# Performance work log

Measured on AMD Instinct MI355X. Metric: run time of the kernel, lower is better.

Reference implementation:

```python
import jax, jax.numpy as jnp
import numpy as np

N_NODES = 100000
IN_CH, HID_CH, OUT_CH = 128, 128, 64
N_EDGES = 1600000


def _gcn_conv(x, W, b, src, dst, num_nodes):
    """PyG GCNConv with gcn_norm(add_self_loops=True): adds one self-loop per
    node to the given edge set, symmetric deg^-1/2 normalization, then
    gather-scale-scatter of the linearly transformed features."""
    loop = jnp.arange(num_nodes)
    s = jnp.concatenate([src, loop])
    d = jnp.concatenate([dst, loop])
    # degree over targets (flow source_to_target), edge weights = 1
    deg = jax.ops.segment_sum(jnp.ones_like(s, x.dtype), d, num_segments=num_nodes)
    dinv = jnp.where(deg > 0, deg ** -0.5, 0.0)
    norm = dinv[s] * dinv[d]                      # [E']
    h = x @ W                                     # [N, out]
    msg = h[s] * norm[:, None]                    # [E', out] gather + scale
    out = jax.ops.segment_sum(msg, d, num_segments=num_nodes)  # scatter-add
    return out + b


def setup_inputs() -> dict:
    key = jax.random.key(0)
    k = jax.random.split(key, 6)
    x = jax.random.normal(k[0], (N_NODES, IN_CH), dtype=jnp.float32)
    edge_index = jax.random.randint(k[1], (2, N_EDGES), 0, N_NODES, dtype=jnp.int64)
    # Glorot-scale params
    W1 = jax.random.normal(k[2], (IN_CH, HID_CH), dtype=jnp.float32) * (2.0 / (IN_CH + HID_CH)) ** 0.5
    b1 = jnp.zeros((HID_CH,), dtype=jnp.float32)
    W2 = jax.random.normal(k[3], (HID_CH, OUT_CH), dtype=jnp.float32) * (2.0 / (HID_CH + OUT_CH)) ** 0.5
    b2 = jnp.zeros((OUT_CH,), dtype=jnp.float32)
    return {"x": x, "edge_index": edge_index, "W1": W1, "b1": b1, "W2": W2, "b2": b2}


def reference(x, edge_index, W1, b1, W2, b2):
    num_nodes = x.shape[0]
    loop = jnp.arange(num_nodes, dtype=edge_index.dtype)
    # wrapper-level add_self_loops (GCNConv adds another internally)
    src = jnp.concatenate([edge_index[0], loop])
    dst = jnp.concatenate([edge_index[1], loop])
    h = _gcn_conv(x, W1, b1, src, dst, num_nodes)
    h = jax.nn.relu(h)
    h = _gcn_conv(h, W2, b2, src, dst, num_nodes)
    return jax.nn.log_softmax(h, axis=1)
```

## Files before the change

### kernel.cpp

```cpp
#include <hip/hip_runtime.h>
#include <cstdint>
#include <cstddef>

#define IN_CH 128
#define HID_CH 128
#define OUT_CH 64
#define BSH 8
#define PB 4096

typedef unsigned int uint32;
typedef unsigned char uchar;
typedef short bf16x8 __attribute__((ext_vector_type(8)));
typedef float f32x4 __attribute__((ext_vector_type(4)));
typedef float f32x2 __attribute__((ext_vector_type(2)));

static __device__ __forceinline__ unsigned short f2bf(float f) {
    uint32 u = __float_as_uint(f);
    u += 0x7fffu + ((u >> 16) & 1u);
    return (unsigned short)(u >> 16);
}
static __device__ __forceinline__ uchar f2fp8(float f) {
    int p = __builtin_amdgcn_cvt_pk_fp8_f32(f, f, 0, false);
    return (uchar)(p & 0xff);
}


__global__ __launch_bounds__(256) void bhist_wtrans(
    const int* __restrict__ dst, int* __restrict__ bcnt, int E, int NB, int gP,
    const float* __restrict__ W1, const float* __restrict__ W2,
    unsigned short* __restrict__ W1t, unsigned short* __restrict__ W2t) {
    if (blockIdx.x >= (uint32)gP) {
        int t = (blockIdx.x - gP) * 256 + threadIdx.x;
        if (t < 128 * 128) {
            int nc = t >> 7, k = t & 127;
            W1t[t] = f2bf(W1[k * 128 + nc]);
        }
        int u = t - 128 * 128;
        if (u >= 0 && u < 64 * 128) {
            int nc = u >> 7, k = u & 127;
            W2t[u] = f2bf(W2[k * 64 + nc]);
        }
        return;
    }
    __shared__ int h[512];
    int t = threadIdx.x;
    int e0 = blockIdx.x * PB;
    int cnt = min(PB, E - e0);
    for (int b = t; b < NB; b += 256) h[b] = 0;
    __syncthreads();
    for (int i = t; i < cnt; i += 256)
        atomicAdd(&h[dst[e0 + i] >> BSH], 1);
    __syncthreads();
    for (int b = t; b < NB; b += 256)
        if (h[b]) atomicAdd(&bcnt[b], h[b]);
}

__global__ void bscan(const int* __restrict__ bcnt, int* __restrict__ bbase,
                      int* __restrict__ bcur, int NB, int E) {
    __shared__ int s[512];
    int t = threadIdx.x;
    int v = (t < NB) ? bcnt[t] : 0;
    s[t] = v;
    __syncthreads();
    for (int o = 1; o < 512; o <<= 1) {
        int add = (t >= o) ? s[t - o] : 0;
        __syncthreads();
        s[t] += add;
        __syncthreads();
    }
    if (t < NB) { bbase[t] = s[t] - v; bcur[t] = 0; }
    if (t == 0) bbase[NB] = E;
}

__global__ __launch_bounds__(256) void part1(
    const int* __restrict__ src, const int* __restrict__ dst,
    const int* __restrict__ bbase, int* __restrict__ bcur,
    int2* __restrict__ pairBuf, int E, int NB) {
    __shared__ int2 pairs[PB];
    __shared__ int hist[512];
    __shared__ int base[512];
    int t = threadIdx.x;
    int e0 = blockIdx.x * PB;
    int cnt = min(PB, E - e0);
    for (int b = t; b < NB; b += 256) hist[b] = 0;
    __syncthreads();
    for (int i = t; i < cnt; i += 256) {
        int s = src[e0 + i], d = dst[e0 + i];
        pairs[i] = make_int2(s, d);
        atomicAdd(&hist[d >> BSH], 1);
    }
    __syncthreads();
    for (int b = t; b < NB; b += 256) {
        int h = hist[b];
        int gb = (h > 0) ? atomicAdd(&bcur[b], h) : 0;
        base[b] = bbase[b] + gb;
        hist[b] = 0;
    }
    __syncthreads();
    for (int i = t; i < cnt; i += 256) {
        int2 p = pairs[i];
        int b = p.y >> BSH;
        int q = base[b] + atomicAdd(&hist[b], 1);
        pairBuf[q] = p;
    }
}

__global__ __launch_bounds__(256) void bucket_build(
    const int2* __restrict__ pairBuf, const int* __restrict__ bbase,
    int* __restrict__ rowptr, int* __restrict__ deg, float* __restrict__ dinv,
    int* __restrict__ csr, int N) {
    __shared__ int cnt[256];
    __shared__ int loc[256];
    int b = blockIdx.x, t = threadIdx.x;
    int start = bbase[b], end = bbase[b + 1];
    cnt[t] = 0;
    __syncthreads();
    for (int i = start + t; i < end; i += 256)
        atomicAdd(&cnt[pairBuf[i].y & 255], 1);
    __syncthreads();
    int v = cnt[t];
    loc[t] = v;
    __syncthreads();
    for (int o = 1; o < 256; o <<= 1) {
        int add = (t >= o) ? loc[t - o] : 0;
        __syncthreads();
        loc[t] += add;
        __syncthreads();
    }
    int excl = loc[t] - v;
    int node = (b << BSH) + t;
    if (node < N) {
        rowptr[node] = start + excl;
        deg[node] = v;
        dinv[node] = rsqrtf((float)(v + 2));
    }
    __syncthreads();
    cnt[t] = excl;
    __syncthreads();
    for (int i = start + t; i < end; i += 256) {
        int2 p = pairBuf[i];
        int q = start + atomicAdd(&cnt[p.y & 255], 1);
        csr[q] = p.x;
    }
}


template <int OUT, bool AFP32>
__global__ __launch_bounds__(256) void gemm_mfma(
    const void* __restrict__ Av, const unsigned short* __restrict__ Wt,
    uchar* __restrict__ C, int n) {
    constexpr int AP = 72;
    constexpr int WP = 136;
    constexpr int NT = OUT / 16;
    __shared__ unsigned short As[128 * AP];
    __shared__ unsigned short Ws[OUT * WP];

    const int t = threadIdx.x;
    const int row0 = blockIdx.x * 128;

    for (int i = t; i < OUT * 16; i += 256) {
        int rr = i >> 4, sq = i & 15;
        *(uint4*)&Ws[rr * WP + sq * 8] = *(const uint4*)(Wt + rr * 128 + sq * 8);
    }

    const int w = t >> 6, l = t & 63;
    const int q = l >> 4, r16 = l & 15;
    const int mbase = w * 32;

    f32x4 acc0[NT], acc1[NT];
    for (int i = 0; i < NT; i++) {
        acc0[i] = (f32x4){0.f, 0.f, 0.f, 0.f};
        acc1[i] = (f32x4){0.f, 0.f, 0.f, 0.f};
    }

    for (int half = 0; half < 2; half++) {
        if (half) __syncthreads();
        if (AFP32) {
            const float* A = (const float*)Av;
            for (int i = t; i < 128 * 16; i += 256) {
                int rr = i >> 4, fq = i & 15;
                float4 v = make_float4(0.f, 0.f, 0.f, 0.f);
                if (row0 + rr < n)
                    v = *(const float4*)(A + (size_t)(row0 + rr) * 128 + half * 64 + fq * 4);
                unsigned short* p = &As[rr * AP + fq * 4];
                p[0] = f2bf(v.x); p[1] = f2bf(v.y); p[2] = f2bf(v.z); p[3] = f2bf(v.w);
            }
        } else {
            const unsigned short* A = (const unsigned short*)Av;
            for (int i = t; i < 128 * 8; i += 256) {
                int rr = i >> 3, sq = i & 7;
                uint4 v = make_uint4(0, 0, 0, 0);
                if (row0 + rr < n)
                    v = *(const uint4*)(A + (size_t)(row0 + rr) * 128 + half * 64 + sq * 8);
                *(uint4*)&As[rr * AP + sq * 8] = v;
            }
        }
        __syncthreads();

#pragma unroll
        for (int kc = 0; kc < 2; kc++) {
            int ko = kc * 32 + q * 8;
            int kow = half * 64 + ko;
            bf16x8 a0 = *(const bf16x8*)&As[(mbase + r16) * AP + ko];
            bf16x8 a1 = *(const bf16x8*)&As[(mbase + 16 + r16) * AP + ko];
#pragma unroll
            for (int nt = 0; nt < NT; nt++) {
                bf16x8 b = *(const bf16x8*)&Ws[(nt * 16 + r16) * WP + kow];
                acc0[nt] = __builtin_amdgcn_mfma_f32_16x16x32_bf16(a0, b, acc0[nt], 0, 0, 0);
                acc1[nt] = __builtin_amdgcn_mfma_f32_16x16x32_bf16(a1, b, acc1[nt], 0, 0, 0);
            }
        }
    }

#pragma unroll
    for (int nt = 0; nt < NT; nt++) {
#pragma unroll
        for (int p = 0; p < 4; p++) {
            int rr = row0 + mbase + q * 4 + p;
            if (rr < n) C[(size_t)rr * OUT + nt * 16 + r16] = f2fp8(acc0[nt][p]);
            if (rr + 16 < n) C[(size_t)(rr + 16) * OUT + nt * 16 + r16] = f2fp8(acc1[nt][p]);
        }
    }
}


__global__ __launch_bounds__(256) void agg_relu_128(
    const uchar* __restrict__ H, const int* __restrict__ csr,
    const int* __restrict__ rowptr, const int* __restrict__ deg,
    const float* __restrict__ dinv, const float* __restrict__ bias,
    unsigned short* __restrict__ out, int n) {
    int v = blockIdx.x * 16 + (threadIdx.x >> 4);
    int hl = threadIdx.x & 15;
    int gsel = threadIdx.x & 48;
    bool valid = v < n;
    int vc = valid ? v : 0;
    int base = rowptr[vc];
    int cnt = valid ? deg[vc] : 0;

    float4 aL0 = make_float4(0.f, 0.f, 0.f, 0.f), aH0 = aL0;
    float4 aL1 = aL0, aH1 = aL0, aL2 = aL0, aH2 = aL0, aL3 = aL0, aH3 = aL0;

    for (int j0 = 0; j0 < cnt; j0 += 16) {
        int nj = min(16, cnt - j0);
        int ul = 0; float wl = 0.f;
        if (hl < nj) { ul = csr[base + j0 + hl]; wl = dinv[ul]; }
        int j = 0;
        for (; j + 4 <= nj; j += 4) {
            int s0 = j | gsel, s1 = (j + 1) | gsel, s2 = (j + 2) | gsel, s3 = (j + 3) | gsel;
            int u0 = __shfl(ul, s0), u1 = __shfl(ul, s1);
            int u2 = __shfl(ul, s2), u3 = __shfl(ul, s3);
            float w0 = __shfl(wl, s0), w1 = __shfl(wl, s1);
            float w2 = __shfl(wl, s2), w3 = __shfl(wl, s3);
            uint2 h0 = *(const uint2*)(H + (size_t)u0 * 128 + hl * 8);
            uint2 h1 = *(const uint2*)(H + (size_t)u1 * 128 + hl * 8);
            uint2 h2 = *(const uint2*)(H + (size_t)u2 * 128 + hl * 8);
            uint2 h3 = *(const uint2*)(H + (size_t)u3 * 128 + hl * 8);
            {
                f32x2 p0 = __builtin_amdgcn_cvt_pk_f32_fp8(h0.x, false);
                f32x2 p1 = __builtin_amdgcn_cvt_pk_f32_fp8(h0.x, true);
                f32x2 p2 = __builtin_amdgcn_cvt_pk_f32_fp8(h0.y, false);
                f32x2 p3 = __builtin_amdgcn_cvt_pk_f32_fp8(h0.y, true);
                aL0.x += w0 * p0[0]; aL0.y += w0 * p0[1]; aL0.z += w0 * p1[0]; aL0.w += w0 * p1[1];
                aH0.x += w0 * p2[0]; aH0.y += w0 * p2[1]; aH0.z += w0 * p3[0]; aH0.w += w0 * p3[1];
            }
            {
                f32x2 p0 = __builtin_amdgcn_cvt_pk_f32_fp8(h1.x, false);
                f32x2 p1 = __builtin_amdgcn_cvt_pk_f32_fp8(h1.x, true);
                f32x2 p2 = __builtin_amdgcn_cvt_pk_f32_fp8(h1.y, false);
                f32x2 p3 = __builtin_amdgcn_cvt_pk_f32_fp8(h1.y, true);
                aL1.x += w1 * p0[0]; aL1.y += w1 * p0[1]; aL1.z += w1 * p1[0]; aL1.w += w1 * p1[1];
                aH1.x += w1 * p2[0]; aH1.y += w1 * p2[1]; aH1.z += w1 * p3[0]; aH1.w += w1 * p3[1];
            }
            {
                f32x2 p0 = __builtin_amdgcn_cvt_pk_f32_fp8(h2.x, false);
                f32x2 p1 = __builtin_amdgcn_cvt_pk_f32_fp8(h2.x, true);
                f32x2 p2 = __builtin_amdgcn_cvt_pk_f32_fp8(h2.y, false);
                f32x2 p3 = __builtin_amdgcn_cvt_pk_f32_fp8(h2.y, true);
                aL2.x += w2 * p0[0]; aL2.y += w2 * p0[1]; aL2.z += w2 * p1[0]; aL2.w += w2 * p1[1];
                aH2.x += w2 * p2[0]; aH2.y += w2 * p2[1]; aH2.z += w2 * p3[0]; aH2.w += w2 * p3[1];
            }
            {
                f32x2 p0 = __builtin_amdgcn_cvt_pk_f32_fp8(h3.x, false);
                f32x2 p1 = __builtin_amdgcn_cvt_pk_f32_fp8(h3.x, true);
                f32x2 p2 = __builtin_amdgcn_cvt_pk_f32_fp8(h3.y, false);
                f32x2 p3 = __builtin_amdgcn_cvt_pk_f32_fp8(h3.y, true);
                aL3.x += w3 * p0[0]; aL3.y += w3 * p0[1]; aL3.z += w3 * p1[0]; aL3.w += w3 * p1[1];
                aH3.x += w3 * p2[0]; aH3.y += w3 * p2[1]; aH3.z += w3 * p3[0]; aH3.w += w3 * p3[1];
            }
        }
        for (; j < nj; j++) {
            int s = j | gsel;
            int u = __shfl(ul, s);
            float wv = __shfl(wl, s);
            uint2 h = *(const uint2*)(H + (size_t)u * 128 + hl * 8);
            f32x2 p0 = __builtin_amdgcn_cvt_pk_f32_fp8(h.x, false);
            f32x2 p1 = __builtin_amdgcn_cvt_pk_f32_fp8(h.x, true);
            f32x2 p2 = __builtin_amdgcn_cvt_pk_f32_fp8(h.y, false);
            f32x2 p3 = __builtin_amdgcn_cvt_pk_f32_fp8(h.y, true);
            aL0.x += wv * p0[0]; aL0.y += wv * p0[1]; aL0.z += wv * p1[0]; aL0.w += wv * p1[1];
            aH0.x += wv * p2[0]; aH0.y += wv * p2[1]; aH0.z += wv * p3[0]; aH0.w += wv * p3[1];
        }
    }
    if (valid) {
        float4 aL = make_float4((aL0.x + aL1.x) + (aL2.x + aL3.x),
                                (aL0.y + aL1.y) + (aL2.y + aL3.y),
                                (aL0.z + aL1.z) + (aL2.z + aL3.z),
                                (aL0.w + aL1.w) + (aL2.w + aL3.w));
        float4 aH = make_float4((aH0.x + aH1.x) + (aH2.x + aH3.x),
                                (aH0.y + aH1.y) + (aH2.y + aH3.y),
                                (aH0.z + aH1.z) + (aH2.z + aH3.z),
                                (aH0.w + aH1.w) + (aH2.w + aH3.w));
        float dv = dinv[vc];
        float sl = 2.f * dv * dv;
        uint2 hv = *(const uint2*)(H + (size_t)vc * 128 + hl * 8);
        f32x2 s0 = __builtin_amdgcn_cvt_pk_f32_fp8(hv.x, false);
        f32x2 s1 = __builtin_amdgcn_cvt_pk_f32_fp8(hv.x, true);
        f32x2 s2 = __builtin_amdgcn_cvt_pk_f32_fp8(hv.y, false);
        f32x2 s3 = __builtin_amdgcn_cvt_pk_f32_fp8(hv.y, true);
        const float4* bp = (const float4*)(bias + hl * 8);
        float4 b0 = bp[0], b1 = bp[1];
        float o0 = fmaxf(dv * aL.x + sl * s0[0] + b0.x, 0.f);
        float o1 = fmaxf(dv * aL.y + sl * s0[1] + b0.y, 0.f);
        float o2 = fmaxf(dv * aL.z + sl * s1[0] + b0.z, 0.f);
        float o3 = fmaxf(dv * aL.w + sl * s1[1] + b0.w, 0.f);
        float o4 = fmaxf(dv * aH.x + sl * s2[0] + b1.x, 0.f);
        float o5 = fmaxf(dv * aH.y + sl * s2[1] + b1.y, 0.f);
        float o6 = fmaxf(dv * aH.z + sl * s3[0] + b1.z, 0.f);
        float o7 = fmaxf(dv * aH.w + sl * s3[1] + b1.w, 0.f);
        uint4 pk;
        pk.x = (uint32)f2bf(o0) | ((uint32)f2bf(o1) << 16);
        pk.y = (uint32)f2bf(o2) | ((uint32)f2bf(o3) << 16);
        pk.z = (uint32)f2bf(o4) | ((uint32)f2bf(o5) << 16);
        pk.w = (uint32)f2bf(o6) | ((uint32)f2bf(o7) << 16);
        *(uint4*)(out + (size_t)vc * 128 + hl * 8) = pk;
    }
}

__global__ __launch_bounds__(256) void agg_lsm_64(
    const uchar* __restrict__ H, const int* __restrict__ csr,
    const int* __restrict__ rowptr, const int* __restrict__ deg,
    const float* __restrict__ dinv, const float* __restrict__ bias,
    float* __restrict__ out, int n) {
    int v = blockIdx.x * 16 + (threadIdx.x >> 4);
    int hl = threadIdx.x & 15;
    int gsel = threadIdx.x & 48;
    bool valid = v < n;
    int vc = valid ? v : 0;
    int base = rowptr[vc];
    int cnt = valid ? deg[vc] : 0;

    float4 a0 = make_float4(0.f, 0.f, 0.f, 0.f), a1 = a0, a2 = a0, a3 = a0;
    for (int j0 = 0; j0 < cnt; j0 += 16) {
        int nj = min(16, cnt - j0);
        int ul = 0; float wl = 0.f;
        if (hl < nj) { ul = csr[base + j0 + hl]; wl = dinv[ul]; }
        int j = 0;
        for (; j + 4 <= nj; j += 4) {
            int s0 = j | gsel, s1 = (j + 1) | gsel, s2 = (j + 2) | gsel, s3 = (j + 3) | gsel;
            int u0 = __shfl(ul, s0), u1 = __shfl(ul, s1);
            int u2 = __shfl(ul, s2), u3 = __shfl(ul, s3);
            float w0 = __shfl(wl, s0), w1 = __shfl(wl, s1);
            float w2 = __shfl(wl, s2), w3 = __shfl(wl, s3);
            uint32 h0 = *(const uint32*)(H + (size_t)u0 * 64 + hl * 4);
            uint32 h1 = *(const uint32*)(H + (size_t)u1 * 64 + hl * 4);
            uint32 h2 = *(const uint32*)(H + (size_t)u2 * 64 + hl * 4);
            uint32 h3 = *(const uint32*)(H + (size_t)u3 * 64 + hl * 4);
            f32x2 l0 = __builtin_amdgcn_cvt_pk_f32_fp8(h0, false);
            f32x2 g0 = __builtin_amdgcn_cvt_pk_f32_fp8(h0, true);
            f32x2 l1 = __builtin_amdgcn_cvt_pk_f32_fp8(h1, false);
            f32x2 g1 = __builtin_amdgcn_cvt_pk_f32_fp8(h1, true);
            f32x2 l2 = __builtin_amdgcn_cvt_pk_f32_fp8(h2, false);
            f32x2 g2 = __builtin_amdgcn_cvt_pk_f32_fp8(h2, true);
            f32x2 l3 = __builtin_amdgcn_cvt_pk_f32_fp8(h3, false);
            f32x2 g3 = __builtin_amdgcn_cvt_pk_f32_fp8(h3, true);
            a0.x += w0 * l0[0]; a0.y += w0 * l0[1]; a0.z += w0 * g0[0]; a0.w += w0 * g0[1];
            a1.x += w1 * l1[0]; a1.y += w1 * l1[1]; a1.z += w1 * g1[0]; a1.w += w1 * g1[1];
            a2.x += w2 * l2[0]; a2.y += w2 * l2[1]; a2.z += w2 * g2[0]; a2.w += w2 * g2[1];
            a3.x += w3 * l3[0]; a3.y += w3 * l3[1]; a3.z += w3 * g3[0]; a3.w += w3 * g3[1];
        }
        for (; j < nj; j++) {
            int s = j | gsel;
            int u = __shfl(ul, s);
            float wv = __shfl(wl, s);
            uint32 h = *(const uint32*)(H + (size_t)u * 64 + hl * 4);
            f32x2 lo = __builtin_amdgcn_cvt_pk_f32_fp8(h, false);
            f32x2 gg = __builtin_amdgcn_cvt_pk_f32_fp8(h, true);
            a0.x += wv * lo[0]; a0.y += wv * lo[1]; a0.z += wv * gg[0]; a0.w += wv * gg[1];
        }
    }
    float4 acc = make_float4((a0.x + a1.x) + (a2.x + a3.x),
                             (a0.y + a1.y) + (a2.y + a3.y),
                             (a0.z + a1.z) + (a2.z + a3.z),
                             (a0.w + a1.w) + (a2.w + a3.w));
    float dv = dinv[vc];
    uint32 hv = *(const uint32*)(H + (size_t)vc * 64 + hl * 4);
    f32x2 dl = __builtin_amdgcn_cvt_pk_f32_fp8(hv, false);
    f32x2 dh = __builtin_amdgcn_cvt_pk_f32_fp8(hv, true);
    float4 bb = ((const float4*)bias)[hl];
    float sl = 2.f * dv * dv;
    float v0 = dv * acc.x + sl * dl[0] + bb.x;
    float v1 = dv * acc.y + sl * dl[1] + bb.y;
    float v2 = dv * acc.z + sl * dh[0] + bb.z;
    float v3 = dv * acc.w + sl * dh[1] + bb.w;
    float m = fmaxf(fmaxf(v0, v1), fmaxf(v2, v3));
    for (int o = 8; o > 0; o >>= 1) m = fmaxf(m, __shfl_xor(m, o));
    float e = (__expf(v0 - m) + __expf(v1 - m)) + (__expf(v2 - m) + __expf(v3 - m));
    for (int o = 8; o > 0; o >>= 1) e += __shfl_xor(e, o);
    float ls = m + __logf(e);
    if (valid)
        *(float4*)(out + (size_t)vc * 64 + hl * 4) =
            make_float4(v0 - ls, v1 - ls, v2 - ls, v3 - ls);
}


extern "C" void kernel_launch(void* const* d_in, const int* in_sizes, int n_in,
                              void* d_out, int out_size, void* d_ws, size_t ws_size,
                              hipStream_t stream) {
    const float* x  = (const float*)d_in[0];
    const int*   ei = (const int*)d_in[1];
    const float* W1 = (const float*)d_in[2];
    const float* b1 = (const float*)d_in[3];
    const float* W2 = (const float*)d_in[4];
    const float* b2 = (const float*)d_in[5];
    float* out = (float*)d_out;

    const int N = in_sizes[0] / IN_CH;
    const int E = in_sizes[1] / 2;
    const int* src = ei;
    const int* dst = ei + E;
    const int NB = (N + 255) >> BSH;

    char* w = (char*)d_ws;
    size_t off = 0;
    auto alloc = [&](size_t bytes) -> char* {
        char* p = w + off;
        off = (off + bytes + 255) & ~(size_t)255;
        return p;
    };
    int*   deg    = (int*)alloc((size_t)N * 4);
    int*   rowptr = (int*)alloc((size_t)N * 4);
    int*   bcnt   = (int*)alloc(512 * 4);
    int*   bbase  = (int*)alloc(513 * 4);
    int*   bcur   = (int*)alloc(512 * 4);
    float* dinv   = (float*)alloc((size_t)N * 4);
    int*   csr    = (int*)alloc((size_t)E * 4);
    unsigned short* W1t = (unsigned short*)alloc(128 * 128 * 2);
    unsigned short* W2t = (unsigned short*)alloc(64 * 128 * 2);
    uchar* H1  = (uchar*)alloc((size_t)N * HID_CH);
    unsigned short* A1b = (unsigned short*)alloc((size_t)N * HID_CH * 2);
    uchar* H2  = H1;
    int2*  pairBuf = (int2*)A1b;

    hipMemsetAsync(bcnt, 0, 512 * 4, stream);

    int gP = (E + PB - 1) / PB;

    bhist_wtrans<<<gP + 96, 256, 0, stream>>>(dst, bcnt, E, NB, gP, W1, W2, W1t, W2t);
    bscan<<<1, 512, 0, stream>>>(bcnt, bbase, bcur, NB, E);
    part1<<<gP, 256, 0, stream>>>(src, dst, bbase, bcur, pairBuf, E, NB);
    bucket_build<<<NB, 256, 0, stream>>>(pairBuf, bbase, rowptr, deg, dinv, csr, N);

    gemm_mfma<128, true><<<(N + 127) / 128, 256, 0, stream>>>(x, W1t, H1, N);
    agg_relu_128<<<(N + 15) / 16, 256, 0, stream>>>(H1, csr, rowptr, deg, dinv, b1, A1b, N);
    gemm_mfma<64, false><<<(N + 127) / 128, 256, 0, stream>>>(A1b, W2t, H2, N);
    agg_lsm_64<<<(N + 15) / 16, 256, 0, stream>>>(H2, csr, rowptr, deg, dinv, b2, out, N);
}
```

Measured before the change: 250.6 us.

## Fold source-side dinv scaling into GEMM epilogue and unroll aggregation by eight

The GEMM epilogue now multiplies each output row by dinv[row] before the fp8 conversion. This lets both aggregation kernels drop the per-neighbor dinv gather and multiply and just sum the fp8-decoded features. The self-loop term becomes dv*2*s, since the stored values already carry dv. The aggregation loops gain an 8-way unroll with packed f32x2 accumulators and 32-bit address arithmetic. The price is a slightly different rounding point for fp8 quantization, and the 32-bit offsets assume N*128 fits in 32 bits.

```diff
diff --git a/kernel.cpp b/kernel.cpp
--- a/kernel.cpp
+++ b/kernel.cpp
@@ -148,7 +148,7 @@
 template <int OUT, bool AFP32>
 __global__ __launch_bounds__(256) void gemm_mfma(
     const void* __restrict__ Av, const unsigned short* __restrict__ Wt,
-    uchar* __restrict__ C, int n) {
+    const float* __restrict__ dinv, uchar* __restrict__ C, int n) {
     constexpr int AP = 72;
     constexpr int WP = 136;
     constexpr int NT = OUT / 16;
@@ -212,13 +212,21 @@
         }
     }
 
+    float dva[4], dvb[4];
+#pragma unroll
+    for (int p = 0; p < 4; p++) {
+        int rr = row0 + mbase + q * 4 + p;
+        dva[p] = (rr < n) ? dinv[rr] : 0.f;
+        dvb[p] = (rr + 16 < n) ? dinv[rr + 16] : 0.f;
+    }
+
 #pragma unroll
     for (int nt = 0; nt < NT; nt++) {
 #pragma unroll
         for (int p = 0; p < 4; p++) {
             int rr = row0 + mbase + q * 4 + p;
-            if (rr < n) C[(size_t)rr * OUT + nt * 16 + r16] = f2fp8(acc0[nt][p]);
-            if (rr + 16 < n) C[(size_t)(rr + 16) * OUT + nt * 16 + r16] = f2fp8(acc1[nt][p]);
+            if (rr < n) C[(size_t)rr * OUT + nt * 16 + r16] = f2fp8(acc0[nt][p] * dva[p]);
+            if (rr + 16 < n) C[(size_t)(rr + 16) * OUT + nt * 16 + r16] = f2fp8(acc1[nt][p] * dvb[p]);
         }
     }
 }
@@ -236,97 +244,82 @@
     int vc = valid ? v : 0;
     int base = rowptr[vc];
     int cnt = valid ? deg[vc] : 0;
-
-    float4 aL0 = make_float4(0.f, 0.f, 0.f, 0.f), aH0 = aL0;
-    float4 aL1 = aL0, aH1 = aL0, aL2 = aL0, aH2 = aL0, aL3 = aL0, aH3 = aL0;
+    const uint32 co = (uint32)(hl * 8);
+
+    f32x2 A0 = (f32x2){0.f, 0.f}, A1 = A0, A2 = A0, A3 = A0;
+    f32x2 B0 = A0, B1 = A0, B2 = A0, B3 = A0;
+
+#define ACC128(h, s0, s1, s2, s3)                                   \
+    {                                                               \
+        s0 += __builtin_amdgcn_cvt_pk_f32_fp8((h).x, false);        \
+        s1 += __builtin_amdgcn_cvt_pk_f32_fp8((h).x, true);         \
+        s2 += __builtin_amdgcn_cvt_pk_f32_fp8((h).y, false);        \
+        s3 += __builtin_amdgcn_cvt_pk_f32_fp8((h).y, true);         \
+    }
 
     for (int j0 = 0; j0 < cnt; j0 += 16) {
         int nj = min(16, cnt - j0);
-        int ul = 0; float wl = 0.f;
-        if (hl < nj) { ul = csr[base + j0 + hl]; wl = dinv[ul]; }
+        int ul = 0;
+        if (hl < nj) ul = csr[base + j0 + hl];
         int j = 0;
+        for (; j + 8 <= nj; j += 8) {
+            int u0 = __shfl(ul, (j + 0) | gsel), u1 = __shfl(ul, (j + 1) | gsel);
+            int u2 = __shfl(ul, (j + 2) | gsel), u3 = __shfl(ul, (j + 3) | gsel);
+            int u4 = __shfl(ul, (j + 4) | gsel), u5 = __shfl(ul, (j + 5) | gsel);
+            int u6 = __shfl(ul, (j + 6) | gsel), u7 = __shfl(ul, (j + 7) | gsel);
+            uint2 h0 = *(const uint2*)(H + (((uint32)u0 << 7) + co));
+            uint2 h1 = *(const uint2*)(H + (((uint32)u1 << 7) + co));
+            uint2 h2 = *(const uint2*)(H + (((uint32)u2 << 7) + co));
+            uint2 h3 = *(const uint2*)(H + (((uint32)u3 << 7) + co));
+            uint2 h4 = *(const uint2*)(H + (((uint32)u4 << 7) + co));
+            uint2 h5 = *(const uint2*)(H + (((uint32)u5 << 7) + co));
+            uint2 h6 = *(const uint2*)(H + (((uint32)u6 << 7) + co));
+            uint2 h7 = *(const uint2*)(H + (((uint32)u7 << 7) + co));
+            ACC128(h0, A0, A1, A2, A3);
+            ACC128(h1, B0, B1, B2, B3);
+            ACC128(h2, A0, A1, A2, A3);
+            ACC128(h3, B0, B1, B2, B3);
+            ACC128(h4, A0, A1, A2, A3);
+            ACC128(h5, B0, B1, B2, B3);
+            ACC128(h6, A0, A1, A2, A3);
+            ACC128(h7, B0, B1, B2, B3);
+        }
         for (; j + 4 <= nj; j += 4) {
-            int s0 = j | gsel, s1 = (j + 1) | gsel, s2 = (j + 2) | gsel, s3 = (j + 3) | gsel;
-            int u0 = __shfl(ul, s0), u1 = __shfl(ul, s1);
-            int u2 = __shfl(ul, s2), u3 = __shfl(ul, s3);
-            float w0 = __shfl(wl, s0), w1 = __shfl(wl, s1);
-            float w2 = __shfl(wl, s2), w3 = __shfl(wl, s3);
-            uint2 h0 = *(const uint2*)(H + (size_t)u0 * 128 + hl * 8);
-            uint2 h1 = *(const uint2*)(H + (size_t)u1 * 128 + hl * 8);
-            uint2 h2 = *(const uint2*)(H + (size_t)u2 * 128 + hl * 8);
-            uint2 h3 = *(const uint2*)(H + (size_t)u3 * 128 + hl * 8);
-            {
-                f32x2 p0 = __builtin_amdgcn_cvt_pk_f32_fp8(h0.x, false);
-                f32x2 p1 = __builtin_amdgcn_cvt_pk_f32_fp8(h0.x, true);
-                f32x2 p2 = __builtin_amdgcn_cvt_pk_f32_fp8(h0.y, false);
-                f32x2 p3 = __builtin_amdgcn_cvt_pk_f32_fp8(h0.y, true);
-                aL0.x += w0 * p0[0]; aL0.y += w0 * p0[1]; aL0.z += w0 * p1[0]; aL0.w += w0 * p1[1];
-                aH0.x += w0 * p2[0]; aH0.y += w0 * p2[1]; aH0.z += w0 * p3[0]; aH0.w += w0 * p3[1];
-            }
-            {
-                f32x2 p0 = __builtin_amdgcn_cvt_pk_f32_fp8(h1.x, false);
-                f32x2 p1 = __builtin_amdgcn_cvt_pk_f32_fp8(h1.x, true);
-                f32x2 p2 = __builtin_amdgcn_cvt_pk_f32_fp8(h1.y, false);
-                f32x2 p3 = __builtin_amdgcn_cvt_pk_f32_fp8(h1.y, true);
-                aL1.x += w1 * p0[0]; aL1.y += w1 * p0[1]; aL1.z += w1 * p1[0]; aL1.w += w1 * p1[1];
-                aH1.x += w1 * p2[0]; aH1.y += w1 * p2[1]; aH1.z += w1 * p3[0]; aH1.w += w1 * p3[1];
-            }
-            {
-                f32x2 p0 = __builtin_amdgcn_cvt_pk_f32_fp8(h2.x, false);
-                f32x2 p1 = __builtin_amdgcn_cvt_pk_f32_fp8(h2.x, true);
-                f32x2 p2 = __builtin_amdgcn_cvt_pk_f32_fp8(h2.y, false);
-                f32x2 p3 = __builtin_amdgcn_cvt_pk_f32_fp8(h2.y, true);
-                aL2.x += w2 * p0[0]; aL2.y += w2 * p0[1]; aL2.z += w2 * p1[0]; aL2.w += w2 * p1[1];
-                aH2.x += w2 * p2[0]; aH2.y += w2 * p2[1]; aH2.z += w2 * p3[0]; aH2.w += w2 * p3[1];
-            }
-            {
-                f32x2 p0 = __builtin_amdgcn_cvt_pk_f32_fp8(h3.x, false);
-                f32x2 p1 = __builtin_amdgcn_cvt_pk_f32_fp8(h3.x, true);
-                f32x2 p2 = __builtin_amdgcn_cvt_pk_f32_fp8(h3.y, false);
-                f32x2 p3 = __builtin_amdgcn_cvt_pk_f32_fp8(h3.y, true);
-                aL3.x += w3 * p0[0]; aL3.y += w3 * p0[1]; aL3.z += w3 * p1[0]; aL3.w += w3 * p1[1];
-                aH3.x += w3 * p2[0]; aH3.y += w3 * p2[1]; aH3.z += w3 * p3[0]; aH3.w += w3 * p3[1];
-            }
+            int u0 = __shfl(ul, (j + 0) | gsel), u1 = __shfl(ul, (j + 1) | gsel);
+            int u2 = __shfl(ul, (j + 2) | gsel), u3 = __shfl(ul, (j + 3) | gsel);
+            uint2 h0 = *(const uint2*)(H + (((uint32)u0 << 7) + co));
+            uint2 h1 = *(const uint2*)(H + (((uint32)u1 << 7) + co));
+            uint2 h2 = *(const uint2*)(H + (((uint32)u2 << 7) + co));
+            uint2 h3 = *(const uint2*)(H + (((uint32)u3 << 7) + co));
+            ACC128(h0, A0, A1, A2, A3);
+            ACC128(h1, B0, B1, B2, B3);
+            ACC128(h2, A0, A1, A2, A3);
+            ACC128(h3, B0, B1, B2, B3);
         }
         for (; j < nj; j++) {
-            int s = j | gsel;
-            int u = __shfl(ul, s);
-            float wv = __shfl(wl, s);
-            uint2 h = *(const uint2*)(H + (size_t)u * 128 + hl * 8);
-            f32x2 p0 = __builtin_amdgcn_cvt_pk_f32_fp8(h.x, false);
-            f32x2 p1 = __builtin_amdgcn_cvt_pk_f32_fp8(h.x, true);
-            f32x2 p2 = __builtin_amdgcn_cvt_pk_f32_fp8(h.y, false);
-            f32x2 p3 = __builtin_amdgcn_cvt_pk_f32_fp8(h.y, true);
-            aL0.x += wv * p0[0]; aL0.y += wv * p0[1]; aL0.z += wv * p1[0]; aL0.w += wv * p1[1];
-            aH0.x += wv * p2[0]; aH0.y += wv * p2[1]; aH0.z += wv * p3[0]; aH0.w += wv * p3[1];
-        }
-    }
+            int u = __shfl(ul, j | gsel);
+            uint2 h = *(const uint2*)(H + (((uint32)u << 7) + co));
+            ACC128(h, A0, A1, A2, A3);
+        }
+    }
+#undef ACC128
+
     if (valid) {
-        float4 aL = make_float4((aL0.x + aL1.x) + (aL2.x + aL3.x),
-                                (aL0.y + aL1.y) + (aL2.y + aL3.y),
-                                (aL0.z + aL1.z) + (aL2.z + aL3.z),
-                                (aL0.w + aL1.w) + (aL2.w + aL3.w));
-        float4 aH = make_float4((aH0.x + aH1.x) + (aH2.x + aH3.x),
-                                (aH0.y + aH1.y) + (aH2.y + aH3.y),
-                                (aH0.z + aH1.z) + (aH2.z + aH3.z),
-                                (aH0.w + aH1.w) + (aH2.w + aH3.w));
         float dv = dinv[vc];
-        float sl = 2.f * dv * dv;
-        uint2 hv = *(const uint2*)(H + (size_t)vc * 128 + hl * 8);
+        uint2 hv = *(const uint2*)(H + (((uint32)vc << 7) + co));
         f32x2 s0 = __builtin_amdgcn_cvt_pk_f32_fp8(hv.x, false);
         f32x2 s1 = __builtin_amdgcn_cvt_pk_f32_fp8(hv.x, true);
         f32x2 s2 = __builtin_amdgcn_cvt_pk_f32_fp8(hv.y, false);
         f32x2 s3 = __builtin_amdgcn_cvt_pk_f32_fp8(hv.y, true);
-        const float4* bp = (const float4*)(bias + hl * 8);
-        float4 b0 = bp[0], b1 = bp[1];
-        float o0 = fmaxf(dv * aL.x + sl * s0[0] + b0.x, 0.f);
-        float o1 = fmaxf(dv * aL.y + sl * s0[1] + b0.y, 0.f);
-        float o2 = fmaxf(dv * aL.z + sl * s1[0] + b0.z, 0.f);
-        float o3 = fmaxf(dv * aL.w + sl * s1[1] + b0.w, 0.f);
-        float o4 = fmaxf(dv * aH.x + sl * s2[0] + b1.x, 0.f);
-        float o5 = fmaxf(dv * aH.y + sl * s2[1] + b1.y, 0.f);
-        float o6 = fmaxf(dv * aH.z + sl * s3[0] + b1.z, 0.f);
-        float o7 = fmaxf(dv * aH.w + sl * s3[1] + b1.w, 0.f);
+        const f32x2* bp = (const f32x2*)(bias + hl * 8);
+        f32x2 e0 = dv * ((A0 + B0) + 2.f * s0) + bp[0];
+        f32x2 e1 = dv * ((A1 + B1) + 2.f * s1) + bp[1];
+        f32x2 e2 = dv * ((A2 + B2) + 2.f * s2) + bp[2];
+        f32x2 e3 = dv * ((A3 + B3) + 2.f * s3) + bp[3];
+        float o0 = fmaxf(e0[0], 0.f), o1 = fmaxf(e0[1], 0.f);
+        float o2 = fmaxf(e1[0], 0.f), o3 = fmaxf(e1[1], 0.f);
+        float o4 = fmaxf(e2[0], 0.f), o5 = fmaxf(e2[1], 0.f);
+        float o6 = fmaxf(e3[0], 0.f), o7 = fmaxf(e3[1], 0.f);
         uint4 pk;
         pk.x = (uint32)f2bf(o0) | ((uint32)f2bf(o1) << 16);
         pk.y = (uint32)f2bf(o2) | ((uint32)f2bf(o3) << 16);
@@ -348,60 +341,71 @@
     int vc = valid ? v : 0;
     int base = rowptr[vc];
     int cnt = valid ? deg[vc] : 0;
-
-    float4 a0 = make_float4(0.f, 0.f, 0.f, 0.f), a1 = a0, a2 = a0, a3 = a0;
+    const uint32 co = (uint32)(hl * 4);
+
+    f32x2 A0 = (f32x2){0.f, 0.f}, A1 = A0, B0 = A0, B1 = A0;
+
+#define ACC64(h, s0, s1)                                            \
+    {                                                               \
+        s0 += __builtin_amdgcn_cvt_pk_f32_fp8((h), false);          \
+        s1 += __builtin_amdgcn_cvt_pk_f32_fp8((h), true);           \
+    }
+
     for (int j0 = 0; j0 < cnt; j0 += 16) {
         int nj = min(16, cnt - j0);
-        int ul = 0; float wl = 0.f;
-        if (hl < nj) { ul = csr[base + j0 + hl]; wl = dinv[ul]; }
+        int ul = 0;
+        if (hl < nj) ul = csr[base + j0 + hl];
         int j = 0;
+        for (; j + 8 <= nj; j += 8) {
+            int u0 = __shfl(ul, (j + 0) | gsel), u1 = __shfl(ul, (j + 1) | gsel);
+            int u2 = __shfl(ul, (j + 2) | gsel), u3 = __shfl(ul, (j + 3) | gsel);
+            int u4 = __shfl(ul, (j + 4) | gsel), u5 = __shfl(ul, (j + 5) | gsel);
+            int u6 = __shfl(ul, (j + 6) | gsel), u7 = __shfl(ul, (j + 7) | gsel);
+            uint32 h0 = *(const uint32*)(H + (((uint32)u0 << 6) + co));
+            uint32 h1 = *(const uint32*)(H + (((uint32)u1 << 6) + co));
+            uint32 h2 = *(const uint32*)(H + (((uint32)u2 << 6) + co));
+            uint32 h3 = *(const uint32*)(H + (((uint32)u3 << 6) + co));
+            uint32 h4 = *(const uint32*)(H + (((uint32)u4 << 6) + co));
+            uint32 h5 = *(const uint32*)(H + (((uint32)u5 << 6) + co));
+            uint32 h6 = *(const uint32*)(H + (((uint32)u6 << 6) + co));
+            uint32 h7 = *(const uint32*)(H + (((uint32)u7 << 6) + co));
+            ACC64(h0, A0, A1);
+            ACC64(h1, B0, B1);
+            ACC64(h2, A0, A1);
+            ACC64(h3, B0, B1);
+            ACC64(h4, A0, A1);
+            ACC64(h5, B0, B1);
+            ACC64(h6, A0, A1);
+            ACC64(h7, B0, B1);
+        }
         for (; j + 4 <= nj; j += 4) {
-            int s0 = j | gsel, s1 = (j + 1) | gsel, s2 = (j + 2) | gsel, s3 = (j + 3) | gsel;
-            int u0 = __shfl(ul, s0), u1 = __shfl(ul, s1);
-            int u2 = __shfl(ul, s2), u3 = __shfl(ul, s3);
-            float w0 = __shfl(wl, s0), w1 = __shfl(wl, s1);
-            float w2 = __shfl(wl, s2), w3 = __shfl(wl, s3);
-            uint32 h0 = *(const uint32*)(H + (size_t)u0 * 64 + hl * 4);
-            uint32 h1 = *(const uint32*)(H + (size_t)u1 * 64 + hl * 4);
-            uint32 h2 = *(const uint32*)(H + (size_t)u2 * 64 + hl * 4);
-            uint32 h3 = *(const uint32*)(H + (size_t)u3 * 64 + hl * 4);
-            f32x2 l0 = __builtin_amdgcn_cvt_pk_f32_fp8(h0, false);
-            f32x2 g0 = __builtin_amdgcn_cvt_pk_f32_fp8(h0, true);
-            f32x2 l1 = __builtin_amdgcn_cvt_pk_f32_fp8(h1, false);
-            f32x2 g1 = __builtin_amdgcn_cvt_pk_f32_fp8(h1, true);
-            f32x2 l2 = __builtin_amdgcn_cvt_pk_f32_fp8(h2, false);
-            f32x2 g2 = __builtin_amdgcn_cvt_pk_f32_fp8(h2, true);
-            f32x2 l3 = __builtin_amdgcn_cvt_pk_f32_fp8(h3, false);
-            f32x2 g3 = __builtin_amdgcn_cvt_pk_f32_fp8(h3, true);
-            a0.x += w0 * l0[0]; a0.y += w0 * l0[1]; a0.z += w0 * g0[0]; a0.w += w0 * g0[1];
-            a1.x += w1 * l1[0]; a1.y += w1 * l1[1]; a1.z += w1 * g1[0]; a1.w += w1 * g1[1];
-            a2.x += w2 * l2[0]; a2.y += w2 * l2[1]; a2.z += w2 * g2[0]; a2.w += w2 * g2[1];
-            a3.x += w3 * l3[0]; a3.y += w3 * l3[1]; a3.z += w3 * g3[0]; a3.w += w3 * g3[1];
+            int u0 = __shfl(ul, (j + 0) | gsel), u1 = __shfl(ul, (j + 1) | gsel);
+            int u2 = __shfl(ul, (j + 2) | gsel), u3 = __shfl(ul, (j + 3) | gsel);
+            uint32 h0 = *(const uint32*)(H + (((uint32)u0 << 6) + co));
+            uint32 h1 = *(const uint32*)(H + (((uint32)u1 << 6) + co));
+            uint32 h2 = *(const uint32*)(H + (((uint32)u2 << 6) + co));
+            uint32 h3 = *(const uint32*)(H + (((uint32)u3 << 6) + co));
+            ACC64(h0, A0, A1);
+            ACC64(h1, B0, B1);
+            ACC64(h2, A0, A1);
+            ACC64(h3, B0, B1);
         }
         for (; j < nj; j++) {
-            int s = j | gsel;
-            int u = __shfl(ul, s);
-            float wv = __shfl(wl, s);
-            uint32 h = *(const uint32*)(H + (size_t)u * 64 + hl * 4);
-            f32x2 lo = __builtin_amdgcn_cvt_pk_f32_fp8(h, false);
-            f32x2 gg = __builtin_amdgcn_cvt_pk_f32_fp8(h, true);
-            a0.x += wv * lo[0]; a0.y += wv * lo[1]; a0.z += wv * gg[0]; a0.w += wv * gg[1];
-        }
-    }
-    float4 acc = make_float4((a0.x + a1.x) + (a2.x + a3.x),
-                             (a0.y + a1.y) + (a2.y + a3.y),
-                             (a0.z + a1.z) + (a2.z + a3.z),
-                             (a0.w + a1.w) + (a2.w + a3.w));
+            int u = __shfl(ul, j | gsel);
+            uint32 h = *(const uint32*)(H + (((uint32)u << 6) + co));
+            ACC64(h, A0, A1);
+        }
+    }
+#undef ACC64
+
     float dv = dinv[vc];
-    uint32 hv = *(const uint32*)(H + (size_t)vc * 64 + hl * 4);
-    f32x2 dl = __builtin_amdgcn_cvt_pk_f32_fp8(hv, false);
-    f32x2 dh = __builtin_amdgcn_cvt_pk_f32_fp8(hv, true);
-    float4 bb = ((const float4*)bias)[hl];
-    float sl = 2.f * dv * dv;
-    float v0 = dv * acc.x + sl * dl[0] + bb.x;
-    float v1 = dv * acc.y + sl * dl[1] + bb.y;
-    float v2 = dv * acc.z + sl * dh[0] + bb.z;
-    float v3 = dv * acc.w + sl * dh[1] + bb.w;
+    uint32 hv = *(const uint32*)(H + (((uint32)vc << 6) + co));
+    f32x2 s0 = __builtin_amdgcn_cvt_pk_f32_fp8(hv, false);
+    f32x2 s1 = __builtin_amdgcn_cvt_pk_f32_fp8(hv, true);
+    const f32x2* bp = (const f32x2*)(bias + hl * 4);
+    f32x2 w0 = dv * ((A0 + B0) + 2.f * s0) + bp[0];
+    f32x2 w1 = dv * ((A1 + B1) + 2.f * s1) + bp[1];
+    float v0 = w0[0], v1 = w0[1], v2 = w1[0], v3 = w1[1];
     float m = fmaxf(fmaxf(v0, v1), fmaxf(v2, v3));
     for (int o = 8; o > 0; o >>= 1) m = fmaxf(m, __shfl_xor(m, o));
     float e = (__expf(v0 - m) + __expf(v1 - m)) + (__expf(v2 - m) + __expf(v3 - m));
@@ -460,8 +464,8 @@
     part1<<<gP, 256, 0, stream>>>(src, dst, bbase, bcur, pairBuf, E, NB);
     bucket_build<<<NB, 256, 0, stream>>>(pairBuf, bbase, rowptr, deg, dinv, csr, N);
 
-    gemm_mfma<128, true><<<(N + 127) / 128, 256, 0, stream>>>(x, W1t, H1, N);
+    gemm_mfma<128, true><<<(N + 127) / 128, 256, 0, stream>>>(x, W1t, dinv, H1, N);
     agg_relu_128<<<(N + 15) / 16, 256, 0, stream>>>(H1, csr, rowptr, deg, dinv, b1, A1b, N);
-    gemm_mfma<64, false><<<(N + 127) / 128, 256, 0, stream>>>(A1b, W2t, H2, N);
+    gemm_mfma<64, false><<<(N + 127) / 128, 256, 0, stream>>>(A1b, W2t, dinv, H2, N);
     agg_lsm_64<<<(N + 15) / 16, 256, 0, stream>>>(H2, csr, rowptr, deg, dinv, b2, out, N);
 }
```

Measured after the change: 261.6 us. +4.4%, slower.
